# Kernel tuning notes

Hardware: AMD Instinct MI355X
Metric: run time of the kernel (lower is better)

## Reference

```python
import jax, jax.numpy as jnp
import numpy as np

B, S, D, H = 32, 128, 64, 4
HD = D // H            # head dim 16
HT = 4 * D             # hidden_t_dim = 256
TE = 4 * HT            # time_embed_dim = 1024
V = 1024               # vocab
STEP = 0.1             # step_size (Lie-Trotter step)


def setup_inputs():
    key = jax.random.key(0)
    ks = jax.random.split(key, 12)
    n = lambda k, shp: 0.02 * jax.random.normal(k, shp, jnp.float32)
    return dict(
        inputs_idx=jax.random.randint(ks[0], (B, S), 0, V),
        num_loops=100,
        wte=n(ks[1], (V, D)),
        wpe=n(ks[2], (S, D)),
        t_w1=n(ks[3], (HT, TE)), t_b1=jnp.zeros((TE,), jnp.float32),
        t_w2=n(ks[4], (TE, D)), t_b2=jnp.zeros((D,), jnp.float32),
        ln1_g=jnp.ones((D,), jnp.float32), ln1_b=jnp.zeros((D,), jnp.float32),
        w_qkv=n(ks[5], (D, 3 * D)), b_qkv=jnp.zeros((3 * D,), jnp.float32),
        w_o=n(ks[6], (D, D)), b_o=jnp.zeros((D,), jnp.float32),
        ln2_g=jnp.ones((D,), jnp.float32), ln2_b=jnp.zeros((D,), jnp.float32),
        w_fc=n(ks[7], (D, 4 * D)), b_fc=jnp.zeros((4 * D,), jnp.float32),
        w_pr=n(ks[8], (4 * D, D)), b_pr=jnp.zeros((D,), jnp.float32),
        lnf_g=jnp.ones((D,), jnp.float32), lnf_b=jnp.zeros((D,), jnp.float32),
    )


def _ln(x, g, b, eps=1e-5):
    mu = jnp.mean(x, axis=-1, keepdims=True)
    var = jnp.var(x, axis=-1, keepdims=True)
    return (x - mu) * jax.lax.rsqrt(var + eps) * g + b


def _timestep_embedding(t, dim):
    # sinusoidal (diffusion-style) embedding of scalar step index t -> (dim,)
    half = dim // 2
    freqs = jnp.exp(-np.log(10000.0) * jnp.arange(half, dtype=jnp.float32) / half)
    args = t * freqs
    return jnp.concatenate([jnp.cos(args), jnp.sin(args)], axis=-1)


def reference(inputs_idx, num_loops, wte, wpe, t_w1, t_b1, t_w2, t_b2,
              ln1_g, ln1_b, w_qkv, b_qkv, w_o, b_o,
              ln2_g, ln2_b, w_fc, b_fc, w_pr, b_pr, lnf_g, lnf_b):
    x = wte[inputs_idx] + wpe[jnp.arange(S)]          # (B,S,D)
    neg_inf = jnp.float32(-1e9)
    cmask = jnp.where(jnp.tril(jnp.ones((S, S), bool)), 0.0, neg_inf)  # causal
    scale = 1.0 / np.sqrt(HD)

    def step(x, t):
        # shared time embedding added to state each loop iteration
        te = _timestep_embedding(t, HT)
        temb = jax.nn.silu(te @ t_w1 + t_b1) @ t_w2 + t_b2   # (D,)
        x = x + temb
        # pre-norm attention, Lie-Trotter sub-step
        h = _ln(x, ln1_g, ln1_b)
        qkv = h @ w_qkv + b_qkv                               # (B,S,3D)
        q, k, v = jnp.split(qkv, 3, axis=-1)
        q = q.reshape(B, S, H, HD)
        k = k.reshape(B, S, H, HD)
        v = v.reshape(B, S, H, HD)
        att = jnp.einsum('bqhd,bkhd->bhqk', q, k) * scale + cmask
        att = jax.nn.softmax(att, axis=-1)
        a = jnp.einsum('bhqk,bkhd->bqhd', att, v).reshape(B, S, D)
        x = x + STEP * (a @ w_o + b_o)
        # pre-norm MLP, second sub-step
        h = _ln(x, ln2_g, ln2_b)
        m = jax.nn.gelu(h @ w_fc + b_fc) @ w_pr + b_pr
        x = x + STEP * m
        return x, None

    ts = jnp.arange(num_loops, dtype=jnp.float32)
    x, _ = jax.lax.scan(step, x, ts)
    return _ln(x, lnf_g, lnf_b)
```

## Files before the change

### kernel.cpp

```cpp
#include <hip/hip_runtime.h>
#include <hip/hip_bf16.h>
#include <math.h>

#define BB   32
#define SS   128
#define DD   64
#define HTT  256
#define TEE  1024
#define NTHR 512
#define STEPF 0.1f

typedef __attribute__((ext_vector_type(8))) short short8b;
typedef __attribute__((ext_vector_type(4))) float float4v;

__device__ __forceinline__ unsigned short f2b(float f) {
    union { float f; unsigned int u; } x; x.f = f;
    unsigned int u = x.u + 0x7FFFu + ((x.u >> 16) & 1u);
    return (unsigned short)(u >> 16);
}
__device__ __forceinline__ unsigned int pack2(float lo, float hi) {
    return (unsigned int)f2b(lo) | ((unsigned int)f2b(hi) << 16);
}

__global__ void pack_frags(const float* __restrict__ w_qkv,
                           const float* __restrict__ w_o,
                           const float* __restrict__ w_fc,
                           const float* __restrict__ w_pr,
                           unsigned short* __restrict__ frags) {
    const int tile = blockIdx.x;
    const int t = threadIdx.x;
    const int lane = t >> 3, e = t & 7;
    const float* W; int N, nt, ks;
    if (tile < 24)      { W = w_qkv; N = 192; int s = tile;      nt = s >> 1; ks = s & 1; }
    else if (tile < 32) { W = w_o;   N = 64;  int s = tile - 24; nt = s >> 1; ks = s & 1; }
    else if (tile < 64) { W = w_fc;  N = 256; int s = tile - 32; nt = s >> 1; ks = s & 1; }
    else                { W = w_pr;  N = 64;  int s = tile - 64; nt = s >> 3; ks = s & 7; }
    const int k   = ks * 32 + (lane >> 4) * 8 + e;
    const int col = nt * 16 + (lane & 15);
    frags[tile * 512 + lane * 8 + e] = f2b(W[k * N + col]);
}

__global__ void temb_precompute(const int* __restrict__ nloops_p,
                                const float* __restrict__ t_w1,
                                const float* __restrict__ t_b1,
                                const float* __restrict__ t_w2,
                                const float* __restrict__ t_b2,
                                float* __restrict__ tembBuf) {
    const int t = blockIdx.x;
    const int nl = nloops_p[0];
    if (t >= nl) return;

    __shared__ float te_s[HTT];
    __shared__ float h1[TEE];
    const int tid = threadIdx.x;
    const float tf = (float)t;

    {
        int fi = (tid < 128) ? tid : (tid - 128);
        float freq = expf(-9.210340371976184f * (float)fi * (1.0f / 128.0f));
        float arg = tf * freq;
        te_s[tid] = (tid < 128) ? cosf(arg) : sinf(arg);
    }
    __syncthreads();

    for (int j = tid; j < TEE; j += 256) {
        float acc = t_b1[j];
        for (int i = 0; i < HTT; ++i)
            acc = fmaf(te_s[i], t_w1[i * TEE + j], acc);
        h1[j] = acc / (1.0f + expf(-acc));
    }
    __syncthreads();

    {
        const int d = tid >> 2, part = tid & 3;
        float acc = 0.0f;
        for (int j = part; j < TEE; j += 4)
            acc = fmaf(h1[j], t_w2[j * DD + d], acc);
        acc += __shfl_xor(acc, 1);
        acc += __shfl_xor(acc, 2);
        if (part == 0) tembBuf[t * DD + d] = acc + t_b2[d];
    }
}

__device__ __forceinline__ float gelu_tanh(float u) {
    float z = 0.7978845608028654f * (u + 0.044715f * u * u * u);
    float e = __expf(2.0f * z);
    float th = 1.0f - 2.0f / (e + 1.0f);
    return 0.5f * u * (1.0f + th);
}

__global__ __launch_bounds__(NTHR, 2)
void looped_tf(const int* __restrict__ idx,
               const int* __restrict__ nloops_p,
               const float* __restrict__ wte,
               const float* __restrict__ wpe,
               const float* __restrict__ ln1_g, const float* __restrict__ ln1_b,
               const float* __restrict__ b_qkv,
               const float* __restrict__ b_o,
               const float* __restrict__ ln2_g, const float* __restrict__ ln2_b,
               const float* __restrict__ b_fc,
               const float* __restrict__ b_pr,
               const float* __restrict__ lnf_g, const float* __restrict__ lnf_b,
               const float* __restrict__ tembBuf,
               const unsigned short* __restrict__ frags,
               float* __restrict__ out) {
    __shared__ __align__(16) unsigned short hsb[SS * DD];
    __shared__ __align__(16) unsigned char pool[66560];
    __shared__ __align__(16) unsigned char pstage[8 * 1152];
    __shared__ __align__(16) unsigned short wfrag[16384];

    unsigned char* qb  = pool;
    unsigned char* kb  = pool + 24576;
    unsigned char* vtb = pool + 49152;
    unsigned short* msb = (unsigned short*)pool;

    const unsigned short* fcF = frags + 32 * 512;
    const unsigned short* prF = frags + 64 * 512;

    const int b   = blockIdx.x;
    const int tid = threadIdx.x;
    const int nl  = nloops_p[0];
    const int wv  = tid >> 6;
    const int ln  = tid & 63;
    const int fr  = ln & 15;
    const int fq  = ln >> 4;
    const int rowbase = wv * 16 + fq * 4;

    for (int i = tid; i < 2048; i += NTHR)
        ((int4*)wfrag)[i] = ((const int4*)frags)[i];

    float bqkvr[12], bor[4], bprr[4];
    float l1g[4], l1b[4], l2g[4], l2b[4], lfg[4], lfb[4];
#pragma unroll
    for (int nt = 0; nt < 12; ++nt) bqkvr[nt] = b_qkv[nt * 16 + fr];
#pragma unroll
    for (int nc = 0; nc < 4; ++nc) {
        int c = nc * 16 + fr;
        bor[nc] = b_o[c];  bprr[nc] = b_pr[c];
        l1g[nc] = ln1_g[c]; l1b[nc] = ln1_b[c];
        l2g[nc] = ln2_g[c]; l2b[nc] = ln2_b[c];
        lfg[nc] = lnf_g[c]; lfb[nc] = lnf_b[c];
    }

    float xr[4][4];
#pragma unroll
    for (int r = 0; r < 4; ++r) {
        int row = rowbase + r;
        int iv = idx[b * SS + row];
#pragma unroll
        for (int nc = 0; nc < 4; ++nc)
            xr[r][nc] = wte[iv * 64 + nc * 16 + fr] + wpe[row * 64 + nc * 16 + fr];
    }

    __syncthreads();

    auto ln_fused = [&](const float* g4, const float* b4) {
        float s1[4], s2[4];
#pragma unroll
        for (int r = 0; r < 4; ++r) {
            s1[r] = xr[r][0] + xr[r][1] + xr[r][2] + xr[r][3];
            s2[r] = xr[r][0]*xr[r][0] + xr[r][1]*xr[r][1]
                  + xr[r][2]*xr[r][2] + xr[r][3]*xr[r][3];
        }
#pragma unroll
        for (int m = 1; m <= 8; m <<= 1) {
#pragma unroll
            for (int r = 0; r < 4; ++r) {
                s1[r] += __shfl_xor(s1[r], m);
                s2[r] += __shfl_xor(s2[r], m);
            }
        }
#pragma unroll
        for (int r = 0; r < 4; ++r) {
            float mu = s1[r] * (1.0f / 64.0f);
            float var = s2[r] * (1.0f / 64.0f) - mu * mu;
            float rs = rsqrtf(var + 1e-5f);
            int row = rowbase + r;
            int swz = (row & 7) << 4;
#pragma unroll
            for (int nc = 0; nc < 4; ++nc) {
                float h = (xr[r][nc] - mu) * rs * g4[nc] + b4[nc];
                int byte = (row * 128 + (nc * 16 + fr) * 2) ^ swz;
                *(unsigned short*)((char*)hsb + byte) = f2b(h);
            }
        }
    };

    auto load_afrag = [&](const unsigned short* buf, int rstrideB, int kstep) -> short8b {
        int row = wv * 16 + fr;
        int byte = row * rstrideB + kstep * 64 + fq * 16;
        return *(const short8b*)((const char*)buf + (byte ^ ((row & 7) << 4)));
    };

    if (nl > 0) {
#pragma unroll
        for (int nc = 0; nc < 4; ++nc) {
            float tv = tembBuf[nc * 16 + fr];
#pragma unroll
            for (int r = 0; r < 4; ++r) xr[r][nc] += tv;
        }
        ln_fused(l1g, l1b);
    }

    for (int t = 0; t < nl; ++t) {
        {
            short8b a0 = load_afrag(hsb, 128, 0);
            short8b a1 = load_afrag(hsb, 128, 1);
            float4v acc[12];
#pragma unroll
            for (int nt = 0; nt < 12; ++nt) acc[nt] = (float4v)0.0f;
#pragma unroll
            for (int nt = 0; nt < 12; ++nt) {
                short8b b0 = *(const short8b*)(&wfrag[(nt * 2 + 0) * 512 + ln * 8]);
                short8b b1 = *(const short8b*)(&wfrag[(nt * 2 + 1) * 512 + ln * 8]);
                acc[nt] = __builtin_amdgcn_mfma_f32_16x16x32_bf16(a0, b0, acc[nt], 0, 0, 0);
                acc[nt] = __builtin_amdgcn_mfma_f32_16x16x32_bf16(a1, b1, acc[nt], 0, 0, 0);
            }
#pragma unroll
            for (int nt = 0; nt < 12; ++nt) {
#pragma unroll
                for (int r = 0; r < 4; ++r) {
                    int row = rowbase + r;
                    unsigned short bv = f2b(acc[nt][r] + bqkvr[nt]);
                    if (nt < 4) {
                        int byte = nt * 6144 + row * 48 + fr * 2;
                        byte ^= ((row >> 3) & 7) << 4;
                        *(unsigned short*)(qb + byte) = bv;
                    } else if (nt < 8) {
                        int h = nt - 4;
                        int p = (row >> 1) + 64 * (row & 1);
                        *(unsigned short*)(kb + h * 6144 + p * 48 + fr * 2) = bv;
                    } else {
                        int h = nt - 8;
                        *(unsigned short*)(vtb + h * 4352 + fr * 272 + row * 2) = bv;
                    }
                }
            }
        }
        __syncthreads();

        {
            short8b aq[4];
            {
                bool lo = (ln < 32);
#pragma unroll
                for (int h = 0; h < 4; ++h) {
                    short8b z = (short8b)(short)0;
                    if (lo) {
                        int q = wv + 8 * fr;
                        int byte = h * 6144 + q * 48 + (fq & 1) * 16;
                        byte ^= (fr & 7) << 4;
                        z = *(const short8b*)(qb + byte);
                    }
                    aq[h] = z;
                }
            }
            short8b onesb;
#pragma unroll
            for (int e = 0; e < 8; ++e) onesb[e] = (short)0x3F80;

            float4v o[4], lac[4];
#pragma unroll
            for (int h = 0; h < 4; ++h) { o[h] = (float4v)0.0f; lac[h] = (float4v)0.0f; }

            unsigned char* pst = pstage + wv * 1152;

            for (int ktp = 0; ktp < 4; ++ktp) {
#pragma unroll
                for (int h = 0; h < 4; ++h) {
                    short8b bk0 = (short8b)(short)0, bk1 = (short8b)(short)0;
                    if (ln < 32) {
                        int kbase = h * 6144 + (fq & 1) * 16;
                        bk0 = *(const short8b*)(kb + kbase + (ktp * 16 + fr) * 48);
                        bk1 = *(const short8b*)(kb + kbase + (64 + ktp * 16 + fr) * 48);
                    }
                    float4v s0 = __builtin_amdgcn_mfma_f32_16x16x32_bf16(aq[h], bk0, (float4v)0.0f, 0, 0, 0);
                    float4v s1 = __builtin_amdgcn_mfma_f32_16x16x32_bf16(aq[h], bk1, (float4v)0.0f, 0, 0, 0);
#pragma unroll
                    for (int r = 0; r < 4; ++r) {
                        int j = 4 * fq + r;
                        int q = wv + 8 * j;
                        int k0 = ktp * 32 + 2 * fr;
                        float p0 = (k0     <= q) ? __expf(s0[r] * 0.25f) : 0.0f;
                        float p1 = (k0 + 1 <= q) ? __expf(s1[r] * 0.25f) : 0.0f;
                        *(unsigned int*)(pst + j * 72 + fr * 4) = pack2(p0, p1);
                    }
                    short8b ap = *(const short8b*)(pst + fr * 72 + fq * 16);
                    short8b bv = *(const short8b*)(vtb + h * 4352 + fr * 272 + ktp * 64 + fq * 16);
                    o[h]   = __builtin_amdgcn_mfma_f32_16x16x32_bf16(ap, bv, o[h], 0, 0, 0);
                    lac[h] = __builtin_amdgcn_mfma_f32_16x16x32_bf16(ap, onesb, lac[h], 0, 0, 0);
                }
            }
#pragma unroll
            for (int h = 0; h < 4; ++h) {
#pragma unroll
                for (int r = 0; r < 4; ++r) {
                    int j = 4 * fq + r;
                    int q = wv + 8 * j;
                    float val = o[h][r] / lac[h][r];
                    int byte = (q * 128 + (h * 16 + fr) * 2) ^ ((q & 7) << 4);
                    *(unsigned short*)((char*)hsb + byte) = f2b(val);
                }
            }
        }
        __syncthreads();

        {
            short8b a0 = load_afrag(hsb, 128, 0);
            short8b a1 = load_afrag(hsb, 128, 1);
            float4v acc[4];
#pragma unroll
            for (int nt = 0; nt < 4; ++nt) acc[nt] = (float4v)0.0f;
#pragma unroll
            for (int nt = 0; nt < 4; ++nt) {
                short8b b0 = *(const short8b*)(&wfrag[(24 + nt * 2 + 0) * 512 + ln * 8]);
                short8b b1 = *(const short8b*)(&wfrag[(24 + nt * 2 + 1) * 512 + ln * 8]);
                acc[nt] = __builtin_amdgcn_mfma_f32_16x16x32_bf16(a0, b0, acc[nt], 0, 0, 0);
                acc[nt] = __builtin_amdgcn_mfma_f32_16x16x32_bf16(a1, b1, acc[nt], 0, 0, 0);
            }
#pragma unroll
            for (int nt = 0; nt < 4; ++nt)
#pragma unroll
                for (int r = 0; r < 4; ++r)
                    xr[r][nt] += STEPF * (acc[nt][r] + bor[nt]);
            ln_fused(l2g, l2b);
        }

        {
            short8b a0 = load_afrag(hsb, 128, 0);
            short8b a1 = load_afrag(hsb, 128, 1);
            float4v acc[16];
#pragma unroll
            for (int nt = 0; nt < 16; ++nt) acc[nt] = (float4v)0.0f;
#pragma unroll
            for (int half = 0; half < 2; ++half) {
                short8b buf[16];
#pragma unroll
                for (int i = 0; i < 16; ++i)
                    buf[i] = *(const short8b*)(fcF + ((half * 16 + i) * 64 + ln) * 8);
#pragma unroll
                for (int i = 0; i < 8; ++i) {
                    int nt = half * 8 + i;
                    acc[nt] = __builtin_amdgcn_mfma_f32_16x16x32_bf16(a0, buf[2*i],   acc[nt], 0, 0, 0);
                    acc[nt] = __builtin_amdgcn_mfma_f32_16x16x32_bf16(a1, buf[2*i+1], acc[nt], 0, 0, 0);
                }
            }
            char* base = (char*)msb;
#pragma unroll
            for (int nt = 0; nt < 16; ++nt) {
                const float bias = b_fc[nt * 16 + fr];
#pragma unroll
                for (int r = 0; r < 4; ++r) {
                    int row = rowbase + r;
                    int byte = row * 512 + (nt * 16 + fr) * 2;
                    *(unsigned short*)(base + (byte ^ ((row & 7) << 4))) =
                        f2b(gelu_tanh(acc[nt][r] + bias));
                }
            }
        }

        {
            short8b am[8];
#pragma unroll
            for (int ks = 0; ks < 8; ++ks)
                am[ks] = load_afrag(msb, 512, ks);
            short8b buf0[16], buf1[16];
#pragma unroll
            for (int i = 0; i < 16; ++i)
                buf0[i] = *(const short8b*)(prF + (i * 64 + ln) * 8);
#pragma unroll
            for (int i = 0; i < 16; ++i)
                buf1[i] = *(const short8b*)(prF + ((16 + i) * 64 + ln) * 8);
            __syncthreads();

            float4v acc[4];
#pragma unroll
            for (int nt = 0; nt < 4; ++nt) acc[nt] = (float4v)0.0f;
#pragma unroll
            for (int i = 0; i < 16; ++i) {
                int nt = i >> 3;
                acc[nt] = __builtin_amdgcn_mfma_f32_16x16x32_bf16(am[i & 7], buf0[i], acc[nt], 0, 0, 0);
            }
#pragma unroll
            for (int i = 0; i < 16; ++i) {
                int nt = 2 + (i >> 3);
                acc[nt] = __builtin_amdgcn_mfma_f32_16x16x32_bf16(am[i & 7], buf1[i], acc[nt], 0, 0, 0);
            }
#pragma unroll
            for (int nt = 0; nt < 4; ++nt)
#pragma unroll
                for (int r = 0; r < 4; ++r)
                    xr[r][nt] += STEPF * (acc[nt][r] + bprr[nt]);

            if (t + 1 < nl) {
#pragma unroll
                for (int nc = 0; nc < 4; ++nc) {
                    float tv = tembBuf[(t + 1) * 64 + nc * 16 + fr];
#pragma unroll
                    for (int r = 0; r < 4; ++r) xr[r][nc] += tv;
                }
                ln_fused(l1g, l1b);
            }
        }
    }

    {
        float s1[4], s2[4];
#pragma unroll
        for (int r = 0; r < 4; ++r) {
            s1[r] = xr[r][0] + xr[r][1] + xr[r][2] + xr[r][3];
            s2[r] = xr[r][0]*xr[r][0] + xr[r][1]*xr[r][1]
                  + xr[r][2]*xr[r][2] + xr[r][3]*xr[r][3];
        }
#pragma unroll
        for (int m = 1; m <= 8; m <<= 1) {
#pragma unroll
            for (int r = 0; r < 4; ++r) {
                s1[r] += __shfl_xor(s1[r], m);
                s2[r] += __shfl_xor(s2[r], m);
            }
        }
#pragma unroll
        for (int r = 0; r < 4; ++r) {
            float mu = s1[r] * (1.0f / 64.0f);
            float var = s2[r] * (1.0f / 64.0f) - mu * mu;
            float rs = rsqrtf(var + 1e-5f);
            int row = rowbase + r;
#pragma unroll
            for (int nc = 0; nc < 4; ++nc) {
                float val = (xr[r][nc] - mu) * rs * lfg[nc] + lfb[nc];
                out[b * SS * DD + row * 64 + nc * 16 + fr] = val;
            }
        }
    }
}

extern "C" void kernel_launch(void* const* d_in, const int* in_sizes, int n_in,
                              void* d_out, int out_size, void* d_ws, size_t ws_size,
                              hipStream_t stream) {
    const int*   idx    = (const int*)  d_in[0];
    const int*   nloops = (const int*)  d_in[1];
    const float* wte    = (const float*)d_in[2];
    const float* wpe    = (const float*)d_in[3];
    const float* t_w1   = (const float*)d_in[4];
    const float* t_b1   = (const float*)d_in[5];
    const float* t_w2   = (const float*)d_in[6];
    const float* t_b2   = (const float*)d_in[7];
    const float* ln1_g  = (const float*)d_in[8];
    const float* ln1_b  = (const float*)d_in[9];
    const float* w_qkv  = (const float*)d_in[10];
    const float* b_qkv  = (const float*)d_in[11];
    const float* w_o    = (const float*)d_in[12];
    const float* b_o    = (const float*)d_in[13];
    const float* ln2_g  = (const float*)d_in[14];
    const float* ln2_b  = (const float*)d_in[15];
    const float* w_fc   = (const float*)d_in[16];
    const float* b_fc   = (const float*)d_in[17];
    const float* w_pr   = (const float*)d_in[18];
    const float* b_pr   = (const float*)d_in[19];
    const float* lnf_g  = (const float*)d_in[20];
    const float* lnf_b  = (const float*)d_in[21];

    float* tembBuf = (float*)d_ws;
    unsigned short* frags = (unsigned short*)((char*)d_ws + 32768);

    pack_frags<<<96, 512, 0, stream>>>(w_qkv, w_o, w_fc, w_pr, frags);
    temb_precompute<<<128, 256, 0, stream>>>(nloops, t_w1, t_b1, t_w2, t_b2, tembBuf);
    looped_tf<<<BB, NTHR, 0, stream>>>(idx, nloops, wte, wpe, ln1_g, ln1_b,
                                       b_qkv, b_o, ln2_g, ln2_b,
                                       b_fc, b_pr, lnf_g, lnf_b,
                                       tembBuf, frags, (float*)d_out);
}
```

Baseline: 3.855 ms.

## Double block to 1024 threads, splitting output columns and heads across wave halves

Doubles the workgroup to 16 waves. Each pair of waves shares a 16-row slice and splits the QKV, attention heads, output projection, MLP columns and residual state between them. LayerNorm statistics now need a cross-wave reduction through shared memory, which adds extra barriers. The aim is more latency hiding and parallel MFMA issue per batch element, since only 32 blocks run. The cost is more synchronisation, duplicated A-fragment loads, and a larger pstage buffer in LDS.

```diff
diff --git a/kernel.cpp b/kernel.cpp
--- a/kernel.cpp
+++ b/kernel.cpp
@@ -7,7 +7,7 @@
 #define DD   64
 #define HTT  256
 #define TEE  1024
-#define NTHR 512
+#define NTHR 1024
 #define STEPF 0.1f
 
 typedef __attribute__((ext_vector_type(8))) short short8b;
@@ -89,7 +89,7 @@
     return 0.5f * u * (1.0f + th);
 }
 
-__global__ __launch_bounds__(NTHR, 2)
+__global__ __launch_bounds__(NTHR, 4)
 void looped_tf(const int* __restrict__ idx,
                const int* __restrict__ nloops_p,
                const float* __restrict__ wte,
@@ -106,8 +106,9 @@
                float* __restrict__ out) {
     __shared__ __align__(16) unsigned short hsb[SS * DD];
     __shared__ __align__(16) unsigned char pool[66560];
-    __shared__ __align__(16) unsigned char pstage[8 * 1152];
+    __shared__ __align__(16) unsigned char pstage[16 * 2 * 1152];
     __shared__ __align__(16) unsigned short wfrag[16384];
+    __shared__ __align__(16) float2 lnred[SS][2];
 
     unsigned char* qb  = pool;
     unsigned char* kb  = pool + 24576;
@@ -121,46 +122,50 @@
     const int tid = threadIdx.x;
     const int nl  = nloops_p[0];
     const int wv  = tid >> 6;
+    const int wg  = wv & 7;
+    const int wh  = wv >> 3;
     const int ln  = tid & 63;
     const int fr  = ln & 15;
     const int fq  = ln >> 4;
-    const int rowbase = wv * 16 + fq * 4;
+    const int rowbase = wg * 16 + fq * 4;
 
     for (int i = tid; i < 2048; i += NTHR)
         ((int4*)wfrag)[i] = ((const int4*)frags)[i];
 
-    float bqkvr[12], bor[4], bprr[4];
-    float l1g[4], l1b[4], l2g[4], l2b[4], lfg[4], lfb[4];
-#pragma unroll
-    for (int nt = 0; nt < 12; ++nt) bqkvr[nt] = b_qkv[nt * 16 + fr];
-#pragma unroll
-    for (int nc = 0; nc < 4; ++nc) {
-        int c = nc * 16 + fr;
+    float bqkvr[6], bfcr[8], bor[2], bprr[2];
+    float l1g[2], l1b[2], l2g[2], l2b[2], lfg[2], lfb[2];
+#pragma unroll
+    for (int i = 0; i < 6; ++i) bqkvr[i] = b_qkv[(wh * 6 + i) * 16 + fr];
+#pragma unroll
+    for (int i = 0; i < 8; ++i) bfcr[i] = b_fc[(wh * 8 + i) * 16 + fr];
+#pragma unroll
+    for (int nc = 0; nc < 2; ++nc) {
+        int c = (wh * 2 + nc) * 16 + fr;
         bor[nc] = b_o[c];  bprr[nc] = b_pr[c];
         l1g[nc] = ln1_g[c]; l1b[nc] = ln1_b[c];
         l2g[nc] = ln2_g[c]; l2b[nc] = ln2_b[c];
         lfg[nc] = lnf_g[c]; lfb[nc] = lnf_b[c];
     }
 
-    float xr[4][4];
+    float xr[4][2];
 #pragma unroll
     for (int r = 0; r < 4; ++r) {
         int row = rowbase + r;
         int iv = idx[b * SS + row];
 #pragma unroll
-        for (int nc = 0; nc < 4; ++nc)
-            xr[r][nc] = wte[iv * 64 + nc * 16 + fr] + wpe[row * 64 + nc * 16 + fr];
-    }
-
+        for (int nc = 0; nc < 2; ++nc) {
+            int c = (wh * 2 + nc) * 16 + fr;
+            xr[r][nc] = wte[iv * 64 + c] + wpe[row * 64 + c];
+        }
+    }
     __syncthreads();
 
-    auto ln_fused = [&](const float* g4, const float* b4) {
+    auto ln_fused = [&](const float* g2, const float* b2) {
         float s1[4], s2[4];
 #pragma unroll
         for (int r = 0; r < 4; ++r) {
-            s1[r] = xr[r][0] + xr[r][1] + xr[r][2] + xr[r][3];
-            s2[r] = xr[r][0]*xr[r][0] + xr[r][1]*xr[r][1]
-                  + xr[r][2]*xr[r][2] + xr[r][3]*xr[r][3];
+            s1[r] = xr[r][0] + xr[r][1];
+            s2[r] = xr[r][0]*xr[r][0] + xr[r][1]*xr[r][1];
         }
 #pragma unroll
         for (int m = 1; m <= 8; m <<= 1) {
@@ -170,32 +175,43 @@
                 s2[r] += __shfl_xor(s2[r], m);
             }
         }
+        if (fr == 0) {
+#pragma unroll
+            for (int r = 0; r < 4; ++r) {
+                float2 v; v.x = s1[r]; v.y = s2[r];
+                lnred[rowbase + r][wh] = v;
+            }
+        }
+        __syncthreads();
 #pragma unroll
         for (int r = 0; r < 4; ++r) {
-            float mu = s1[r] * (1.0f / 64.0f);
-            float var = s2[r] * (1.0f / 64.0f) - mu * mu;
+            float2 oth = lnred[rowbase + r][wh ^ 1];
+            float t1 = s1[r] + oth.x, t2 = s2[r] + oth.y;
+            float mu = t1 * (1.0f / 64.0f);
+            float var = t2 * (1.0f / 64.0f) - mu * mu;
             float rs = rsqrtf(var + 1e-5f);
             int row = rowbase + r;
             int swz = (row & 7) << 4;
 #pragma unroll
-            for (int nc = 0; nc < 4; ++nc) {
-                float h = (xr[r][nc] - mu) * rs * g4[nc] + b4[nc];
-                int byte = (row * 128 + (nc * 16 + fr) * 2) ^ swz;
+            for (int nc = 0; nc < 2; ++nc) {
+                float h = (xr[r][nc] - mu) * rs * g2[nc] + b2[nc];
+                int byte = (row * 128 + ((wh * 2 + nc) * 16 + fr) * 2) ^ swz;
                 *(unsigned short*)((char*)hsb + byte) = f2b(h);
             }
         }
+        __syncthreads();
     };
 
     auto load_afrag = [&](const unsigned short* buf, int rstrideB, int kstep) -> short8b {
-        int row = wv * 16 + fr;
+        int row = wg * 16 + fr;
         int byte = row * rstrideB + kstep * 64 + fq * 16;
         return *(const short8b*)((const char*)buf + (byte ^ ((row & 7) << 4)));
     };
 
     if (nl > 0) {
 #pragma unroll
-        for (int nc = 0; nc < 4; ++nc) {
-            float tv = tembBuf[nc * 16 + fr];
+        for (int nc = 0; nc < 2; ++nc) {
+            float tv = tembBuf[(wh * 2 + nc) * 16 + fr];
 #pragma unroll
             for (int r = 0; r < 4; ++r) xr[r][nc] += tv;
         }
@@ -206,22 +222,24 @@
         {
             short8b a0 = load_afrag(hsb, 128, 0);
             short8b a1 = load_afrag(hsb, 128, 1);
-            float4v acc[12];
-#pragma unroll
-            for (int nt = 0; nt < 12; ++nt) acc[nt] = (float4v)0.0f;
-#pragma unroll
-            for (int nt = 0; nt < 12; ++nt) {
+            float4v acc[6];
+#pragma unroll
+            for (int i = 0; i < 6; ++i) acc[i] = (float4v)0.0f;
+#pragma unroll
+            for (int i = 0; i < 6; ++i) {
+                int nt = wh * 6 + i;
                 short8b b0 = *(const short8b*)(&wfrag[(nt * 2 + 0) * 512 + ln * 8]);
                 short8b b1 = *(const short8b*)(&wfrag[(nt * 2 + 1) * 512 + ln * 8]);
-                acc[nt] = __builtin_amdgcn_mfma_f32_16x16x32_bf16(a0, b0, acc[nt], 0, 0, 0);
-                acc[nt] = __builtin_amdgcn_mfma_f32_16x16x32_bf16(a1, b1, acc[nt], 0, 0, 0);
-            }
-#pragma unroll
-            for (int nt = 0; nt < 12; ++nt) {
+                acc[i] = __builtin_amdgcn_mfma_f32_16x16x32_bf16(a0, b0, acc[i], 0, 0, 0);
+                acc[i] = __builtin_amdgcn_mfma_f32_16x16x32_bf16(a1, b1, acc[i], 0, 0, 0);
+            }
+#pragma unroll
+            for (int i = 0; i < 6; ++i) {
+                int nt = wh * 6 + i;
 #pragma unroll
                 for (int r = 0; r < 4; ++r) {
                     int row = rowbase + r;
-                    unsigned short bv = f2b(acc[nt][r] + bqkvr[nt]);
+                    unsigned short bv = f2b(acc[i][r] + bqkvr[i]);
                     if (nt < 4) {
                         int byte = nt * 6144 + row * 48 + fr * 2;
                         byte ^= ((row >> 3) & 7) << 4;
@@ -240,46 +258,45 @@
         __syncthreads();
 
         {
-            short8b aq[4];
-            {
-                bool lo = (ln < 32);
-#pragma unroll
-                for (int h = 0; h < 4; ++h) {
-                    short8b z = (short8b)(short)0;
+            const bool lo = (ln < 32);
+            short8b aq[2];
+#pragma unroll
+            for (int hh = 0; hh < 2; ++hh) {
+                int h = wh * 2 + hh;
+                short8b z = (short8b)(short)0;
+                if (lo) {
+                    int q = wg + 8 * fr;
+                    int byte = h * 6144 + q * 48 + (fq & 1) * 16;
+                    byte ^= (fr & 7) << 4;
+                    z = *(const short8b*)(qb + byte);
+                }
+                aq[hh] = z;
+            }
+            short8b onesb;
+#pragma unroll
+            for (int e = 0; e < 8; ++e) onesb[e] = (short)0x3F80;
+
+            float4v o[2], lac[2];
+#pragma unroll
+            for (int hh = 0; hh < 2; ++hh) { o[hh] = (float4v)0.0f; lac[hh] = (float4v)0.0f; }
+
+            for (int ktp = 0; ktp < 4; ++ktp) {
+#pragma unroll
+                for (int hh = 0; hh < 2; ++hh) {
+                    int h = wh * 2 + hh;
+                    unsigned char* pst = pstage + (wv * 2 + hh) * 1152;
+                    short8b bk0 = (short8b)(short)0, bk1 = (short8b)(short)0;
                     if (lo) {
-                        int q = wv + 8 * fr;
-                        int byte = h * 6144 + q * 48 + (fq & 1) * 16;
-                        byte ^= (fr & 7) << 4;
-                        z = *(const short8b*)(qb + byte);
-                    }
-                    aq[h] = z;
-                }
-            }
-            short8b onesb;
-#pragma unroll
-            for (int e = 0; e < 8; ++e) onesb[e] = (short)0x3F80;
-
-            float4v o[4], lac[4];
-#pragma unroll
-            for (int h = 0; h < 4; ++h) { o[h] = (float4v)0.0f; lac[h] = (float4v)0.0f; }
-
-            unsigned char* pst = pstage + wv * 1152;
-
-            for (int ktp = 0; ktp < 4; ++ktp) {
-#pragma unroll
-                for (int h = 0; h < 4; ++h) {
-                    short8b bk0 = (short8b)(short)0, bk1 = (short8b)(short)0;
-                    if (ln < 32) {
                         int kbase = h * 6144 + (fq & 1) * 16;
                         bk0 = *(const short8b*)(kb + kbase + (ktp * 16 + fr) * 48);
                         bk1 = *(const short8b*)(kb + kbase + (64 + ktp * 16 + fr) * 48);
                     }
-                    float4v s0 = __builtin_amdgcn_mfma_f32_16x16x32_bf16(aq[h], bk0, (float4v)0.0f, 0, 0, 0);
-                    float4v s1 = __builtin_amdgcn_mfma_f32_16x16x32_bf16(aq[h], bk1, (float4v)0.0f, 0, 0, 0);
+                    float4v s0 = __builtin_amdgcn_mfma_f32_16x16x32_bf16(aq[hh], bk0, (float4v)0.0f, 0, 0, 0);
+                    float4v s1 = __builtin_amdgcn_mfma_f32_16x16x32_bf16(aq[hh], bk1, (float4v)0.0f, 0, 0, 0);
 #pragma unroll
                     for (int r = 0; r < 4; ++r) {
                         int j = 4 * fq + r;
-                        int q = wv + 8 * j;
+                        int q = wg + 8 * j;
                         int k0 = ktp * 32 + 2 * fr;
                         float p0 = (k0     <= q) ? __expf(s0[r] * 0.25f) : 0.0f;
                         float p1 = (k0 + 1 <= q) ? __expf(s1[r] * 0.25f) : 0.0f;
@@ -287,17 +304,18 @@
                     }
                     short8b ap = *(const short8b*)(pst + fr * 72 + fq * 16);
                     short8b bv = *(const short8b*)(vtb + h * 4352 + fr * 272 + ktp * 64 + fq * 16);
-                    o[h]   = __builtin_amdgcn_mfma_f32_16x16x32_bf16(ap, bv, o[h], 0, 0, 0);
-                    lac[h] = __builtin_amdgcn_mfma_f32_16x16x32_bf16(ap, onesb, lac[h], 0, 0, 0);
-                }
-            }
-#pragma unroll
-            for (int h = 0; h < 4; ++h) {
+                    o[hh]   = __builtin_amdgcn_mfma_f32_16x16x32_bf16(ap, bv, o[hh], 0, 0, 0);
+                    lac[hh] = __builtin_amdgcn_mfma_f32_16x16x32_bf16(ap, onesb, lac[hh], 0, 0, 0);
+                }
+            }
+#pragma unroll
+            for (int hh = 0; hh < 2; ++hh) {
+                int h = wh * 2 + hh;
 #pragma unroll
                 for (int r = 0; r < 4; ++r) {
                     int j = 4 * fq + r;
-                    int q = wv + 8 * j;
-                    float val = o[h][r] / lac[h][r];
+                    int q = wg + 8 * j;
+                    float val = o[hh][r] / lac[hh][r];
                     int byte = (q * 128 + (h * 16 + fr) * 2) ^ ((q & 7) << 4);
                     *(unsigned short*)((char*)hsb + byte) = f2b(val);
                 }
@@ -308,94 +326,81 @@
         {
             short8b a0 = load_afrag(hsb, 128, 0);
             short8b a1 = load_afrag(hsb, 128, 1);
-            float4v acc[4];
-#pragma unroll
-            for (int nt = 0; nt < 4; ++nt) acc[nt] = (float4v)0.0f;
-#pragma unroll
-            for (int nt = 0; nt < 4; ++nt) {
+            float4v acc[2];
+#pragma unroll
+            for (int i = 0; i < 2; ++i) acc[i] = (float4v)0.0f;
+#pragma unroll
+            for (int i = 0; i < 2; ++i) {
+                int nt = wh * 2 + i;
                 short8b b0 = *(const short8b*)(&wfrag[(24 + nt * 2 + 0) * 512 + ln * 8]);
                 short8b b1 = *(const short8b*)(&wfrag[(24 + nt * 2 + 1) * 512 + ln * 8]);
-                acc[nt] = __builtin_amdgcn_mfma_f32_16x16x32_bf16(a0, b0, acc[nt], 0, 0, 0);
-                acc[nt] = __builtin_amdgcn_mfma_f32_16x16x32_bf16(a1, b1, acc[nt], 0, 0, 0);
-            }
-#pragma unroll
-            for (int nt = 0; nt < 4; ++nt)
+                acc[i] = __builtin_amdgcn_mfma_f32_16x16x32_bf16(a0, b0, acc[i], 0, 0, 0);
+                acc[i] = __builtin_amdgcn_mfma_f32_16x16x32_bf16(a1, b1, acc[i], 0, 0, 0);
+            }
+#pragma unroll
+            for (int i = 0; i < 2; ++i)
 #pragma unroll
                 for (int r = 0; r < 4; ++r)
-                    xr[r][nt] += STEPF * (acc[nt][r] + bor[nt]);
+                    xr[r][i] += STEPF * (acc[i][r] + bor[i]);
             ln_fused(l2g, l2b);
         }
 
         {
             short8b a0 = load_afrag(hsb, 128, 0);
             short8b a1 = load_afrag(hsb, 128, 1);
-            float4v acc[16];
-#pragma unroll
-            for (int nt = 0; nt < 16; ++nt) acc[nt] = (float4v)0.0f;
-#pragma unroll
-            for (int half = 0; half < 2; ++half) {
-                short8b buf[16];
-#pragma unroll
-                for (int i = 0; i < 16; ++i)
-                    buf[i] = *(const short8b*)(fcF + ((half * 16 + i) * 64 + ln) * 8);
-#pragma unroll
-                for (int i = 0; i < 8; ++i) {
-                    int nt = half * 8 + i;
-                    acc[nt] = __builtin_amdgcn_mfma_f32_16x16x32_bf16(a0, buf[2*i],   acc[nt], 0, 0, 0);
-                    acc[nt] = __builtin_amdgcn_mfma_f32_16x16x32_bf16(a1, buf[2*i+1], acc[nt], 0, 0, 0);
-                }
+            float4v acc[8];
+#pragma unroll
+            for (int i = 0; i < 8; ++i) acc[i] = (float4v)0.0f;
+#pragma unroll
+            for (int i = 0; i < 8; ++i) {
+                int nt = wh * 8 + i;
+                short8b b0 = *(const short8b*)(fcF + ((nt * 2 + 0) * 64 + ln) * 8);
+                short8b b1 = *(const short8b*)(fcF + ((nt * 2 + 1) * 64 + ln) * 8);
+                acc[i] = __builtin_amdgcn_mfma_f32_16x16x32_bf16(a0, b0, acc[i], 0, 0, 0);
+                acc[i] = __builtin_amdgcn_mfma_f32_16x16x32_bf16(a1, b1, acc[i], 0, 0, 0);
             }
             char* base = (char*)msb;
 #pragma unroll
-            for (int nt = 0; nt < 16; ++nt) {
-                const float bias = b_fc[nt * 16 + fr];
+            for (int i = 0; i < 8; ++i) {
+                int nt = wh * 8 + i;
 #pragma unroll
                 for (int r = 0; r < 4; ++r) {
                     int row = rowbase + r;
                     int byte = row * 512 + (nt * 16 + fr) * 2;
                     *(unsigned short*)(base + (byte ^ ((row & 7) << 4))) =
-                        f2b(gelu_tanh(acc[nt][r] + bias));
-                }
-            }
-        }
+                        f2b(gelu_tanh(acc[i][r] + bfcr[i]));
+                }
+            }
+        }
+        __syncthreads();
 
         {
             short8b am[8];
 #pragma unroll
             for (int ks = 0; ks < 8; ++ks)
                 am[ks] = load_afrag(msb, 512, ks);
-            short8b buf0[16], buf1[16];
-#pragma unroll
-            for (int i = 0; i < 16; ++i)
-                buf0[i] = *(const short8b*)(prF + (i * 64 + ln) * 8);
-#pragma unroll
-            for (int i = 0; i < 16; ++i)
-                buf1[i] = *(const short8b*)(prF + ((16 + i) * 64 + ln) * 8);
-            __syncthreads();
-
-            float4v acc[4];
-#pragma unroll
-            for (int nt = 0; nt < 4; ++nt) acc[nt] = (float4v)0.0f;
-#pragma unroll
-            for (int i = 0; i < 16; ++i) {
-                int nt = i >> 3;
-                acc[nt] = __builtin_amdgcn_mfma_f32_16x16x32_bf16(am[i & 7], buf0[i], acc[nt], 0, 0, 0);
-            }
-#pragma unroll
-            for (int i = 0; i < 16; ++i) {
-                int nt = 2 + (i >> 3);
-                acc[nt] = __builtin_amdgcn_mfma_f32_16x16x32_bf16(am[i & 7], buf1[i], acc[nt], 0, 0, 0);
-            }
-#pragma unroll
-            for (int nt = 0; nt < 4; ++nt)
+            float4v acc[2];
+#pragma unroll
+            for (int i = 0; i < 2; ++i) acc[i] = (float4v)0.0f;
+#pragma unroll
+            for (int i = 0; i < 2; ++i) {
+                int nt = wh * 2 + i;
+#pragma unroll
+                for (int ks = 0; ks < 8; ++ks) {
+                    short8b bp = *(const short8b*)(prF + ((nt * 8 + ks) * 64 + ln) * 8);
+                    acc[i] = __builtin_amdgcn_mfma_f32_16x16x32_bf16(am[ks], bp, acc[i], 0, 0, 0);
+                }
+            }
+#pragma unroll
+            for (int i = 0; i < 2; ++i)
 #pragma unroll
                 for (int r = 0; r < 4; ++r)
-                    xr[r][nt] += STEPF * (acc[nt][r] + bprr[nt]);
+                    xr[r][i] += STEPF * (acc[i][r] + bprr[i]);
 
             if (t + 1 < nl) {
 #pragma unroll
-                for (int nc = 0; nc < 4; ++nc) {
-                    float tv = tembBuf[(t + 1) * 64 + nc * 16 + fr];
+                for (int nc = 0; nc < 2; ++nc) {
+                    float tv = tembBuf[(t + 1) * 64 + (wh * 2 + nc) * 16 + fr];
 #pragma unroll
                     for (int r = 0; r < 4; ++r) xr[r][nc] += tv;
                 }
@@ -408,9 +413,8 @@
         float s1[4], s2[4];
 #pragma unroll
         for (int r = 0; r < 4; ++r) {
-            s1[r] = xr[r][0] + xr[r][1] + xr[r][2] + xr[r][3];
-            s2[r] = xr[r][0]*xr[r][0] + xr[r][1]*xr[r][1]
-                  + xr[r][2]*xr[r][2] + xr[r][3]*xr[r][3];
+            s1[r] = xr[r][0] + xr[r][1];
+            s2[r] = xr[r][0]*xr[r][0] + xr[r][1]*xr[r][1];
         }
 #pragma unroll
         for (int m = 1; m <= 8; m <<= 1) {
@@ -420,16 +424,26 @@
                 s2[r] += __shfl_xor(s2[r], m);
             }
         }
+        if (fr == 0) {
+#pragma unroll
+            for (int r = 0; r < 4; ++r) {
+                float2 v; v.x = s1[r]; v.y = s2[r];
+                lnred[rowbase + r][wh] = v;
+            }
+        }
+        __syncthreads();
 #pragma unroll
         for (int r = 0; r < 4; ++r) {
-            float mu = s1[r] * (1.0f / 64.0f);
-            float var = s2[r] * (1.0f / 64.0f) - mu * mu;
+            float2 oth = lnred[rowbase + r][wh ^ 1];
+            float t1 = s1[r] + oth.x, t2 = s2[r] + oth.y;
+            float mu = t1 * (1.0f / 64.0f);
+            float var = t2 * (1.0f / 64.0f) - mu * mu;
             float rs = rsqrtf(var + 1e-5f);
             int row = rowbase + r;
 #pragma unroll
-            for (int nc = 0; nc < 4; ++nc) {
-                float val = (xr[r][nc] - mu) * rs * lfg[nc] + lfb[nc];
-                out[b * SS * DD + row * 64 + nc * 16 + fr] = val;
+            for (int nc = 0; nc < 2; ++nc) {
+                int c = (wh * 2 + nc) * 16 + fr;
+                out[b * SS * DD + row * 64 + c] = (xr[r][nc] - mu) * rs * lfg[nc] + lfb[nc];
             }
         }
     }
```

After: 3.504 ms. 1.1x faster.
